# Performance work log

Measured on AMD Instinct MI355X. Metric: run time of the kernel, lower is better.

## Reference

```python
import jax, jax.numpy as jnp
import numpy as np
from jax import lax

B, T, I, H = 32, 512, 512, 1024


def setup_inputs() -> dict:
    key = jax.random.key(0)
    k0, k1, k2, k3, k4 = jax.random.split(key, 5)
    s_i = 1.0 / np.sqrt(I).astype(np.float32)
    s_h = 1.0 / np.sqrt(H).astype(np.float32)
    x = jax.random.normal(k0, (B, T, I), dtype=jnp.float32)
    # stacked gate weights, order: input(i), forget(f), cell(g), output(o)
    Wx = jax.random.uniform(k1, (4 * H, I), jnp.float32, -s_i, s_i)
    bx = jax.random.uniform(k2, (4 * H,), jnp.float32, -s_i, s_i)
    Wh = jax.random.uniform(k3, (4 * H, H), jnp.float32, -s_h, s_h)
    bh = jax.random.uniform(k4, (4 * H,), jnp.float32, -s_h, s_h)
    return {"x": x, "Wx": Wx, "bx": bx, "Wh": Wh, "bh": bh}


def reference(x, Wx, bx, Wh, bh):
    # Pre-compute all input-to-gate projections in one batched GEMM: [B,T,4H]
    xg = jnp.einsum("bti,gi->btg", x, Wx) + bx + bh

    def step(carry, xg_t):
        h, c = carry
        gates = xg_t + h @ Wh.T  # [B,4H]
        i, f, g, o = jnp.split(gates, 4, axis=-1)
        i = jax.nn.sigmoid(i)
        f = jax.nn.sigmoid(f)
        g = jnp.tanh(g)
        o = jax.nn.sigmoid(o)
        c = f * c + i * g
        h = o * jnp.tanh(c)  # r is None in forward -> h_tilde = tanh(c)
        return (h, c), h

    b = x.shape[0]
    h0 = jnp.zeros((b, H), dtype=x.dtype)
    c0 = jnp.zeros((b, H), dtype=x.dtype)
    _, hs = lax.scan(step, (h0, c0), jnp.swapaxes(xg, 0, 1))  # hs: [T,B,H]
    return jnp.swapaxes(hs, 0, 1)  # [B,T,H]
```

## Files before the change

### kernel.cpp

```cpp
#include <hip/hip_runtime.h>
#include <hip/hip_bf16.h>

#define Bv 32
#define Tv 512
#define Iv 512
#define Hv 1024
#define NG 4096

typedef short bf16x8 __attribute__((ext_vector_type(8)));
typedef float floatx16 __attribute__((ext_vector_type(16)));
typedef unsigned short u16;
typedef unsigned int u32;
typedef unsigned long long u64;
typedef u32 u32x4 __attribute__((ext_vector_type(4)));

__device__ __forceinline__ u16 f2bf(float f) {
  __hip_bfloat16 h = __float2bfloat16(f);
  return *reinterpret_cast<u16*>(&h);
}

__device__ __forceinline__ floatx16 mfma32(bf16x8 a, bf16x8 b, floatx16 c) {
  return __builtin_amdgcn_mfma_f32_32x32x16_bf16(a, b, c, 0, 0, 0);
}

__device__ __forceinline__ bf16x8 as_bf16x8(u32x4 v) {
  union { u32x4 u; bf16x8 b; } c; c.u = v; return c.b;
}

__device__ __forceinline__ u64 ld_agent_u64(const u64* p) {
  return __hip_atomic_load(p, __ATOMIC_RELAXED, __HIP_MEMORY_SCOPE_AGENT);
}
__device__ __forceinline__ void st_agent_u16(u16* p, u16 v) {
  __hip_atomic_store(p, v, __ATOMIC_RELAXED, __HIP_MEMORY_SCOPE_AGENT);
}

__device__ __forceinline__ bf16x8 mk_frag(u64 lo, u64 hi) {
  union { u64 q[2]; bf16x8 v; } u;
  u.q[0] = lo; u.q[1] = hi;
  return u.v;
}

__global__ void k_init(unsigned int* p, int n) {
  int i = blockIdx.x * blockDim.x + threadIdx.x;
  if (i < n) p[i] = 0u;
}

__global__ void k_f2bf(const float* __restrict__ in, u16* __restrict__ out, int n) {
  int i = blockIdx.x * blockDim.x + threadIdx.x;
  if (i < n) out[i] = f2bf(in[i]);
}

__global__ void k_whf(const float* __restrict__ Wh, u16* __restrict__ whf) {
  int tid = blockIdx.x * 256 + threadIdx.x;
  int lane = tid & 63;
  int kt   = (tid >> 6) & 63;
  int nt   = (tid >> 12) & 1;
  int bl   = tid >> 13;
  int r    = nt * 32 + (lane & 31);
  int gate = r >> 4, du = r & 15;
  int row  = gate * Hv + bl * 16 + du;
  int k0   = kt * 16 + (lane >> 5) * 8;
  const float* s = Wh + (size_t)row * Hv + k0;
  u16* d = whf + (size_t)tid * 8;
#pragma unroll
  for (int j = 0; j < 8; ++j) d[j] = f2bf(s[j]);
}

__global__ __launch_bounds__(256) void k_xg(const u16* __restrict__ xb, const u16* __restrict__ wxb,
                                            const float* __restrict__ bx, const float* __restrict__ bh,
                                            float* __restrict__ xg, int t0, int tcshift) {
  __shared__ u16 Al[128 * 40];
  __shared__ u16 Bl[128 * 40];
  int tid = threadIdx.x;
  int wave = tid >> 6, lane = tid & 63;
  int wm = wave & 1, wn = wave >> 1;
  int bm = blockIdx.x, bn = blockIdx.y;
  int Tc = 1 << tcshift;

  floatx16 acc[2][2];
#pragma unroll
  for (int a = 0; a < 2; ++a)
#pragma unroll
    for (int c = 0; c < 2; ++c)
#pragma unroll
      for (int r = 0; r < 16; ++r) acc[a][c][r] = 0.f;

  int lr = tid >> 1;
  int lk = (tid & 1) * 16;
  int m  = bm * 128 + lr;
  int b  = m >> tcshift;
  int tl = m & (Tc - 1);
  const u16* asrc = xb + (size_t)(b * Tv + t0 + tl) * Iv + lk;
  int nrow = bn * 128 + lr;
  const u16* bsrc = wxb + (size_t)nrow * Iv + lk;
  u16* adst = &Al[lr * 40 + lk];
  u16* bdst = &Bl[lr * 40 + lk];

  for (int k0 = 0; k0 < Iv; k0 += 32) {
    __syncthreads();
    *(uint4*)adst       = *(const uint4*)(asrc);
    *(uint4*)(adst + 8) = *(const uint4*)(asrc + 8);
    *(uint4*)bdst       = *(const uint4*)(bsrc);
    *(uint4*)(bdst + 8) = *(const uint4*)(bsrc + 8);
    asrc += 32; bsrc += 32;
    __syncthreads();
#pragma unroll
    for (int kt = 0; kt < 2; ++kt) {
      int ko = kt * 16 + (lane >> 5) * 8;
      bf16x8 a0 = *(const bf16x8*)(&Al[(wm * 64 +      (lane & 31)) * 40 + ko]);
      bf16x8 a1 = *(const bf16x8*)(&Al[(wm * 64 + 32 + (lane & 31)) * 40 + ko]);
      bf16x8 b0 = *(const bf16x8*)(&Bl[(wn * 64 +      (lane & 31)) * 40 + ko]);
      bf16x8 b1 = *(const bf16x8*)(&Bl[(wn * 64 + 32 + (lane & 31)) * 40 + ko]);
      acc[0][0] = mfma32(a0, b0, acc[0][0]);
      acc[0][1] = mfma32(a0, b1, acc[0][1]);
      acc[1][0] = mfma32(a1, b0, acc[1][0]);
      acc[1][1] = mfma32(a1, b1, acc[1][1]);
    }
  }
#pragma unroll
  for (int mt = 0; mt < 2; ++mt) {
#pragma unroll
    for (int ntt = 0; ntt < 2; ++ntt) {
      int nGl = bn * 128 + wn * 64 + ntt * 32 + (lane & 31);
      float bias = bx[nGl] + bh[nGl];
#pragma unroll
      for (int r = 0; r < 16; ++r) {
        int mrow = (r & 3) + 8 * (r >> 2) + 4 * (lane >> 5);
        int mG = bm * 128 + wm * 64 + mt * 32 + mrow;
        int bb = mG >> tcshift;
        int tt = mG & (Tc - 1);
        xg[((size_t)(tt * Bv + bb) << 12) + nGl] = acc[mt][ntt][r] + bias;
      }
    }
  }
}

__global__ __launch_bounds__(256, 1) void k_scan(const u16* __restrict__ whf, const float* __restrict__ xg,
                                                 u64* __restrict__ hA, float* __restrict__ cbuf,
                                                 float* __restrict__ out, int* arrivals, int t0, int Tc) {
  __shared__ float red[2][4][64][36];
  __shared__ float obuf[16][2][16][16];
  int tid = threadIdx.x;
  int bl = blockIdx.x;
  int kh = tid >> 6, lane = tid & 63;
  int eu = tid & 15, eb = tid >> 4;
  int u0 = bl * 16;

  u32x4 w[32];
  {
    const u16* wb0 = whf + ((size_t)(bl * 2 + 0) << 15);
    const u16* wb1 = whf + ((size_t)(bl * 2 + 1) << 15);
#pragma unroll
    for (int kk = 0; kk < 16; ++kk) {
      int kt = kh * 16 + kk;
      asm volatile("global_load_dwordx4 %0, %1, off" : "=v"(w[kk])
                   : "v"(wb0 + (size_t)((kt << 6) + lane) * 8));
      asm volatile("global_load_dwordx4 %0, %1, off" : "=v"(w[kk + 16])
                   : "v"(wb1 + (size_t)((kt << 6) + lane) * 8));
    }
    asm volatile("s_waitcnt vmcnt(0)" ::: "memory");
    __builtin_amdgcn_sched_barrier(0);
  }

  float c0, c1;
  if (t0 == 0) { c0 = 0.f; c1 = 0.f; }
  else {
    c0 = cbuf[eb * Hv + u0 + eu];
    c1 = cbuf[(eb + 16) * Hv + u0 + eu];
  }

  u16* hA16 = (u16*)hA;
  const int* fp = arrivals + ((kh << 4) + (lane & 15)) * 16;

  float xgv[4][2];
#pragma unroll
  for (int g = 0; g < 4; ++g)
#pragma unroll
    for (int b2 = 0; b2 < 2; ++b2)
      xgv[g][b2] = xg[((size_t)(0 * Bv + eb + 16 * b2) << 12) + g * Hv + u0 + eu];

  for (int tl = 0; tl < Tc; ++tl) {
    int t = t0 + tl;

    while (__hip_atomic_load(fp, __ATOMIC_RELAXED, __HIP_MEMORY_SCOPE_AGENT) < t) { }
    asm volatile("" ::: "memory");

    const u64* hAr = hA + (size_t)(t & 1) * 8192;

    u64 alo[16], ahi[16];
#pragma unroll
    for (int kk = 0; kk < 16; ++kk) {
      size_t fi = (size_t)((((kh << 4) + kk) << 6) + lane) * 2;
      alo[kk] = ld_agent_u64(hAr + fi);
      ahi[kk] = ld_agent_u64(hAr + fi + 1);
    }

    float xgn[4][2];
    {
      int tln = (tl + 1 < Tc) ? tl + 1 : tl;
#pragma unroll
      for (int g = 0; g < 4; ++g)
#pragma unroll
        for (int b2 = 0; b2 < 2; ++b2)
          xgn[g][b2] = xg[((size_t)(tln * Bv + eb + 16 * b2) << 12) + g * Hv + u0 + eu];
    }

    floatx16 acc0, acc1;
#pragma unroll
    for (int r = 0; r < 16; ++r) { acc0[r] = 0.f; acc1[r] = 0.f; }
#pragma unroll
    for (int kk = 0; kk < 16; ++kk) {
      bf16x8 a = mk_frag(alo[kk], ahi[kk]);
      acc0 = mfma32(a, as_bf16x8(w[kk]),      acc0);
      acc1 = mfma32(a, as_bf16x8(w[kk + 16]), acc1);
    }

    {
      int n = lane & 31;
      int bq = 4 * (lane >> 5);
#pragma unroll
      for (int rq = 0; rq < 4; ++rq) {
        float4 v0 = make_float4(acc0[rq * 4 + 0], acc0[rq * 4 + 1], acc0[rq * 4 + 2], acc0[rq * 4 + 3]);
        float4 v1 = make_float4(acc1[rq * 4 + 0], acc1[rq * 4 + 1], acc1[rq * 4 + 2], acc1[rq * 4 + 3]);
        *(float4*)&red[t & 1][kh][n][8 * rq + bq]      = v0;
        *(float4*)&red[t & 1][kh][32 + n][8 * rq + bq] = v1;
      }
    }

    __syncthreads();

    float hv0, hv1;
    {
      float gs[4][2];
#pragma unroll
      for (int g = 0; g < 4; ++g) {
        int r = g * 16 + eu;
#pragma unroll
        for (int b2 = 0; b2 < 2; ++b2) {
          int b = eb + 16 * b2;
          gs[g][b2] = red[t & 1][0][r][b] + red[t & 1][1][r][b] +
                      red[t & 1][2][r][b] + red[t & 1][3][r][b] + xgv[g][b2];
        }
      }
      float i0 = 1.f / (1.f + __expf(-gs[0][0]));
      float f0 = 1.f / (1.f + __expf(-gs[1][0]));
      float g0 = 1.f - 2.f / (__expf(2.f * gs[2][0]) + 1.f);
      float o0 = 1.f / (1.f + __expf(-gs[3][0]));
      c0 = f0 * c0 + i0 * g0;
      hv0 = o0 * (1.f - 2.f / (__expf(2.f * c0) + 1.f));

      float i1 = 1.f / (1.f + __expf(-gs[0][1]));
      float f1 = 1.f / (1.f + __expf(-gs[1][1]));
      float g1 = 1.f - 2.f / (__expf(2.f * gs[2][1]) + 1.f);
      float o1 = 1.f / (1.f + __expf(-gs[3][1]));
      c1 = f1 * c1 + i1 * g1;
      hv1 = o1 * (1.f - 2.f / (__expf(2.f * c1) + 1.f));
    }

    {
      int ts = tl & 15;
      obuf[ts][0][eb][eu] = hv0;
      obuf[ts][1][eb][eu] = hv1;
    }

    u16* hAw16 = hA16 + (size_t)((t + 1) & 1) * 32768;
    st_agent_u16(hAw16 + ((size_t)((bl << 6) + eb +      ((eu >> 3) << 5)) << 3) + (eu & 7), f2bf(hv0));
    st_agent_u16(hAw16 + ((size_t)((bl << 6) + eb + 16 + ((eu >> 3) << 5)) << 3) + (eu & 7), f2bf(hv1));
    asm volatile("s_waitcnt vmcnt(0)" ::: "memory");
    __syncthreads();

    if (tid == 0)
      __hip_atomic_store(arrivals + bl * 16, t + 1, __ATOMIC_RELAXED, __HIP_MEMORY_SCOPE_AGENT);

    if ((tl & 15) == 15 || tl == Tc - 1) {
      int ns = (tl & 15) + 1;
      int tb = t - (tl & 15);
      for (int ts = 0; ts < ns; ++ts) {
        out[((size_t)(eb * Tv + tb + ts) << 10) + u0 + eu]        = obuf[ts][0][eb][eu];
        out[((size_t)((eb + 16) * Tv + tb + ts) << 10) + u0 + eu] = obuf[ts][1][eb][eu];
      }
    }

#pragma unroll
    for (int g = 0; g < 4; ++g)
#pragma unroll
      for (int b2 = 0; b2 < 2; ++b2) xgv[g][b2] = xgn[g][b2];
  }
  cbuf[eb * Hv + u0 + eu] = c0;
  cbuf[(eb + 16) * Hv + u0 + eu] = c1;
}

extern "C" void kernel_launch(void* const* d_in, const int* in_sizes, int n_in,
                              void* d_out, int out_size, void* d_ws, size_t ws_size,
                              hipStream_t stream) {
  const float* x  = (const float*)d_in[0];
  const float* Wx = (const float*)d_in[1];
  const float* bx = (const float*)d_in[2];
  const float* Wh = (const float*)d_in[3];
  const float* bh = (const float*)d_in[4];
  float* out = (float*)d_out;
  char* ws = (char*)d_ws;

  int*   arrivals = (int*)ws;
  u64*   hA  = (u64*)(ws + 4096);
  float* cb  = (float*)(ws + 4096 + (128 << 10));
  u16*   xb  = (u16*)(ws + 4096 + (256 << 10));
  u16*   wxb = xb + (size_t)Bv * Tv * Iv;
  u16*   whf = wxb + (size_t)NG * Iv;
  float* xg  = (float*)(whf + (size_t)64 * 2 * 64 * 64 * 8);

  size_t fixedB = 4096 + (256ull << 10) +
                  ((size_t)Bv * Tv * Iv + (size_t)NG * Iv + (size_t)64 * 2 * 64 * 64 * 8) * 2;
  int tcshift = 9;
  while (tcshift > 2 && fixedB + (((size_t)Bv * NG * 4) << tcshift) > ws_size) --tcshift;
  int Tc = 1 << tcshift;

  k_init<<<132, 256, 0, stream>>>((unsigned int*)ws, (4096 + (128 << 10)) / 4);
  k_f2bf<<<(Bv * Tv * Iv) / 256, 256, 0, stream>>>(x, xb, Bv * Tv * Iv);
  k_f2bf<<<(NG * Iv) / 256, 256, 0, stream>>>(Wx, wxb, NG * Iv);
  k_whf<<<2048, 256, 0, stream>>>(Wh, whf);

  for (int t0 = 0; t0 < Tv; t0 += Tc) {
    k_xg<<<dim3(Tc / 4, 32), 256, 0, stream>>>(xb, wxb, bx, bh, xg, t0, tcshift);
    k_scan<<<64, 256, 0, stream>>>(whf, xg, hA, cb, out, arrivals, t0, Tc);
  }
}
```

Before: 2.396 ms.

## Store gate projections in bf16 and overlap next-chunk GEMM with the scan

The precomputed input projections xg are now stored as bf16 instead of fp32. This halves the bytes written by the GEMM and read by the recurrent scan at every step. The scan kernel also launches extra blocks beyond the 64 recurrent ones; these compute the next time-chunk's projection GEMM into a double buffer while the scan runs, so the separate per-chunk GEMM launches go away. The trade-offs are reduced precision in the gate inputs and more register and scheduling pressure in the combined kernel. The overlap only applies when the workspace forces more than one chunk.

```diff
diff --git a/kernel.cpp b/kernel.cpp
--- a/kernel.cpp
+++ b/kernel.cpp
@@ -17,6 +17,9 @@
 __device__ __forceinline__ u16 f2bf(float f) {
   __hip_bfloat16 h = __float2bfloat16(f);
   return *reinterpret_cast<u16*>(&h);
+}
+__device__ __forceinline__ float bf2f(u16 v) {
+  union { u32 u; float f; } c; c.u = ((u32)v) << 16; return c.f;
 }
 
 __device__ __forceinline__ floatx16 mfma32(bf16x8 a, bf16x8 b, floatx16 c) {
@@ -68,7 +71,7 @@
 
 __global__ __launch_bounds__(256) void k_xg(const u16* __restrict__ xb, const u16* __restrict__ wxb,
                                             const float* __restrict__ bx, const float* __restrict__ bh,
-                                            float* __restrict__ xg, int t0, int tcshift) {
+                                            u16* __restrict__ xg, int t0, int tcshift) {
   __shared__ u16 Al[128 * 40];
   __shared__ u16 Bl[128 * 40];
   int tid = threadIdx.x;
@@ -129,18 +132,91 @@
         int mG = bm * 128 + wm * 64 + mt * 32 + mrow;
         int bb = mG >> tcshift;
         int tt = mG & (Tc - 1);
-        xg[((size_t)(tt * Bv + bb) << 12) + nGl] = acc[mt][ntt][r] + bias;
-      }
-    }
-  }
-}
-
-__global__ __launch_bounds__(256, 1) void k_scan(const u16* __restrict__ whf, const float* __restrict__ xg,
+        xg[((size_t)(tt * Bv + bb) << 12) + nGl] = f2bf(acc[mt][ntt][r] + bias);
+      }
+    }
+  }
+}
+
+__global__ __launch_bounds__(256, 1) void k_scan(const u16* __restrict__ whf, const u16* __restrict__ xg,
+                                                 u16* __restrict__ xgN,
+                                                 const float* __restrict__ bx, const float* __restrict__ bh,
+                                                 const u16* __restrict__ xb, const u16* __restrict__ wxb,
                                                  u64* __restrict__ hA, float* __restrict__ cbuf,
-                                                 float* __restrict__ out, int* arrivals, int t0, int Tc) {
+                                                 float* __restrict__ out, int* arrivals,
+                                                 int t0, int Tc, int tcshift) {
   __shared__ float red[2][4][64][36];
   __shared__ float obuf[16][2][16][16];
   int tid = threadIdx.x;
+
+  if (blockIdx.x >= 64) {
+    int t0n = t0 + Tc;
+    if (t0n >= Tv) return;
+    u16* Al = (u16*)red;
+    u16* Bl = Al + 128 * 40;
+    int wave = tid >> 6, lane = tid & 63;
+    int wm = wave & 1, wn = wave >> 1;
+    int lr = tid >> 1;
+    int lk = (tid & 1) * 16;
+    int ntiles = (((Bv << tcshift) >> 7) << 5);
+    for (int tile = (int)blockIdx.x - 64; tile < ntiles; tile += 192) {
+      int bm = tile >> 5, bn = tile & 31;
+      floatx16 acc[2][2];
+#pragma unroll
+      for (int a = 0; a < 2; ++a)
+#pragma unroll
+        for (int c = 0; c < 2; ++c)
+#pragma unroll
+          for (int r = 0; r < 16; ++r) acc[a][c][r] = 0.f;
+      int m  = bm * 128 + lr;
+      int b  = m >> tcshift;
+      int tl = m & (Tc - 1);
+      const u16* asrc = xb + (size_t)(b * Tv + t0n + tl) * Iv + lk;
+      const u16* bsrc = wxb + (size_t)(bn * 128 + lr) * Iv + lk;
+      u16* adst = &Al[lr * 40 + lk];
+      u16* bdst = &Bl[lr * 40 + lk];
+      for (int k0 = 0; k0 < Iv; k0 += 32) {
+        __syncthreads();
+        *(uint4*)adst       = *(const uint4*)(asrc);
+        *(uint4*)(adst + 8) = *(const uint4*)(asrc + 8);
+        *(uint4*)bdst       = *(const uint4*)(bsrc);
+        *(uint4*)(bdst + 8) = *(const uint4*)(bsrc + 8);
+        asrc += 32; bsrc += 32;
+        __syncthreads();
+#pragma unroll
+        for (int kt = 0; kt < 2; ++kt) {
+          int ko = kt * 16 + (lane >> 5) * 8;
+          bf16x8 a0 = *(const bf16x8*)(&Al[(wm * 64 +      (lane & 31)) * 40 + ko]);
+          bf16x8 a1 = *(const bf16x8*)(&Al[(wm * 64 + 32 + (lane & 31)) * 40 + ko]);
+          bf16x8 b0 = *(const bf16x8*)(&Bl[(wn * 64 +      (lane & 31)) * 40 + ko]);
+          bf16x8 b1 = *(const bf16x8*)(&Bl[(wn * 64 + 32 + (lane & 31)) * 40 + ko]);
+          acc[0][0] = mfma32(a0, b0, acc[0][0]);
+          acc[0][1] = mfma32(a0, b1, acc[0][1]);
+          acc[1][0] = mfma32(a1, b0, acc[1][0]);
+          acc[1][1] = mfma32(a1, b1, acc[1][1]);
+        }
+      }
+#pragma unroll
+      for (int mt = 0; mt < 2; ++mt) {
+#pragma unroll
+        for (int ntt = 0; ntt < 2; ++ntt) {
+          int nGl = bn * 128 + wn * 64 + ntt * 32 + (lane & 31);
+          float bias = bx[nGl] + bh[nGl];
+#pragma unroll
+          for (int r = 0; r < 16; ++r) {
+            int mrow = (r & 3) + 8 * (r >> 2) + 4 * (lane >> 5);
+            int mG = bm * 128 + wm * 64 + mt * 32 + mrow;
+            int bb = mG >> tcshift;
+            int tt = mG & (Tc - 1);
+            xgN[((size_t)(tt * Bv + bb) << 12) + nGl] = f2bf(acc[mt][ntt][r] + bias);
+          }
+        }
+      }
+      __syncthreads();
+    }
+    return;
+  }
+
   int bl = blockIdx.x;
   int kh = tid >> 6, lane = tid & 63;
   int eu = tid & 15, eb = tid >> 4;
@@ -172,7 +248,7 @@
   u16* hA16 = (u16*)hA;
   const int* fp = arrivals + ((kh << 4) + (lane & 15)) * 16;
 
-  float xgv[4][2];
+  u16 xgv[4][2];
 #pragma unroll
   for (int g = 0; g < 4; ++g)
 #pragma unroll
@@ -195,7 +271,7 @@
       ahi[kk] = ld_agent_u64(hAr + fi + 1);
     }
 
-    float xgn[4][2];
+    u16 xgn[4][2];
     {
       int tln = (tl + 1 < Tc) ? tl + 1 : tl;
 #pragma unroll
@@ -239,7 +315,7 @@
         for (int b2 = 0; b2 < 2; ++b2) {
           int b = eb + 16 * b2;
           gs[g][b2] = red[t & 1][0][r][b] + red[t & 1][1][r][b] +
-                      red[t & 1][2][r][b] + red[t & 1][3][r][b] + xgv[g][b2];
+                      red[t & 1][2][r][b] + red[t & 1][3][r][b] + bf2f(xgv[g][b2]);
         }
       }
       float i0 = 1.f / (1.f + __expf(-gs[0][0]));
@@ -307,7 +383,6 @@
   u16*   xb  = (u16*)(ws + 4096 + (256 << 10));
   u16*   wxb = xb + (size_t)Bv * Tv * Iv;
   u16*   whf = wxb + (size_t)NG * Iv;
-  float* xg  = (float*)(whf + (size_t)64 * 2 * 64 * 64 * 8);
 
   size_t fixedB = 4096 + (256ull << 10) +
                   ((size_t)Bv * Tv * Iv + (size_t)NG * Iv + (size_t)64 * 2 * 64 * 64 * 8) * 2;
@@ -315,13 +390,22 @@
   while (tcshift > 2 && fixedB + (((size_t)Bv * NG * 4) << tcshift) > ws_size) --tcshift;
   int Tc = 1 << tcshift;
 
+  u16* xg0 = whf + (size_t)64 * 2 * 64 * 64 * 8;
+  u16* xg1 = xg0 + (((size_t)Bv * NG) << tcshift);
+
   k_init<<<132, 256, 0, stream>>>((unsigned int*)ws, (4096 + (128 << 10)) / 4);
   k_f2bf<<<(Bv * Tv * Iv) / 256, 256, 0, stream>>>(x, xb, Bv * Tv * Iv);
   k_f2bf<<<(NG * Iv) / 256, 256, 0, stream>>>(Wx, wxb, NG * Iv);
   k_whf<<<2048, 256, 0, stream>>>(Wh, whf);
 
-  for (int t0 = 0; t0 < Tv; t0 += Tc) {
-    k_xg<<<dim3(Tc / 4, 32), 256, 0, stream>>>(xb, wxb, bx, bh, xg, t0, tcshift);
-    k_scan<<<64, 256, 0, stream>>>(whf, xg, hA, cb, out, arrivals, t0, Tc);
-  }
-}
+  k_xg<<<dim3(Tc / 4, 32), 256, 0, stream>>>(xb, wxb, bx, bh, xg0, 0, tcshift);
+
+  int c = 0;
+  for (int t0 = 0; t0 < Tv; t0 += Tc, ++c) {
+    u16* cur = (c & 1) ? xg1 : xg0;
+    u16* nxt = (c & 1) ? xg0 : xg1;
+    bool more = (t0 + Tc) < Tv;
+    k_scan<<<more ? 256 : 64, 256, 0, stream>>>(whf, cur, nxt, bx, bh, xb, wxb,
+                                                hA, cb, out, arrivals, t0, Tc, tcshift);
+  }
+}
```

Result: no change. 2.410 ms (+0.6%).
